# Kernel tuning notes

Measured on AMD Instinct MI355X. Metric: run time of the kernel, lower is better.

## Reference

```python
import jax, jax.numpy as jnp
import numpy as np

N_NODES = 50000
N_EDGES = 800000
D = 64
L = 3


def setup_inputs() -> dict:
    key = jax.random.key(0)
    ks = jax.random.split(key, 6)
    glorot = (6.0 / (D + D)) ** 0.5  # xavier_uniform bound for [D,D]
    return {
        "x": jax.random.normal(ks[0], (N_NODES, D), dtype=jnp.float32),
        "edge_index": jax.random.randint(ks[1], (2, N_EDGES), 0, N_NODES, dtype=jnp.int32),
        "edge_weight": jax.random.uniform(ks[2], (N_EDGES,), dtype=jnp.float32),
        "W_rel": jax.random.uniform(ks[3], (L, D, D), jnp.float32, -glorot, glorot),
        "b_rel": jnp.zeros((L, D), dtype=jnp.float32),
        "W_root": jax.random.uniform(ks[4], (L, D, D), jnp.float32, -glorot, glorot),
    }


def reference(x, edge_index, edge_weight, W_rel, b_rel, W_root):
    """myGNN_hidden.full_forward final embedding: L GraphConv(add) layers, tanh on last.
    GraphConv: h_i' = h_i @ W_root + (sum_{j->i} e_ji * h_j) @ W_rel + b_rel.
    """
    src, dst = edge_index[0], edge_index[1]
    n = x.shape[0]
    h = x
    num_layers = W_rel.shape[0]
    for i in range(num_layers):
        msg = edge_weight[:, None] * h[src]                      # [E, D] gather + scale
        agg = jax.ops.segment_sum(msg, dst, num_segments=n)      # [N, D] scatter-add
        h = agg @ W_rel[i] + b_rel[i] + h @ W_root[i]
        if i == num_layers - 1:
            h = jnp.tanh(h)
    return h
```

## Files before the change

### kernel.cpp

```cpp
#include <hip/hip_runtime.h>
#include <hip/hip_bf16.h>

#define NN 50000
#define NE 800000
#define DD 64
#define NL 3
#define NE_PAD (NE + NN * 8)

__device__ __forceinline__ float rlane(float v, int l) {
    return __int_as_float(__builtin_amdgcn_readlane(__float_as_int(v), l));
}

__global__ void hist_kernel(const int* __restrict__ dst,
                            int* __restrict__ deg,
                            int* __restrict__ rank) {
    int t = blockIdx.x * blockDim.x + threadIdx.x;
    int e = t * 4;
    if (e + 4 <= NE) {
        int4 d4 = *reinterpret_cast<const int4*>(dst + e);
        int r0 = atomicAdd(&deg[d4.x], 1);
        int r1 = atomicAdd(&deg[d4.y], 1);
        int r2 = atomicAdd(&deg[d4.z], 1);
        int r3 = atomicAdd(&deg[d4.w], 1);
        *reinterpret_cast<int4*>(rank + e) = make_int4(r0, r1, r2, r3);
    } else {
        for (int i = e; i < NE; ++i) rank[i] = atomicAdd(&deg[dst[i]], 1);
    }
}

__global__ void alloc_kernel(const int* __restrict__ deg,
                             int* __restrict__ row_start,
                             int* __restrict__ counter) {
    int n = blockIdx.x * blockDim.x + threadIdx.x;
    int lane = threadIdx.x & 63;
    int d = (n < NN) ? ((deg[n] + 7) & ~7) : 0;
    int s = d;
    #pragma unroll
    for (int off = 1; off < 64; off <<= 1) {
        int t = __shfl_up(s, off);
        if (lane >= off) s += t;
    }
    int total = __shfl(s, 63);
    int base = 0;
    if (lane == 63) base = atomicAdd(counter, total);
    base = __shfl(base, 63);
    int my = base + s - d;
    if (n < NN) row_start[n] = my;
}

__global__ void reorder_kernel(const int* __restrict__ src,
                               const int* __restrict__ dst,
                               const float* __restrict__ w,
                               const int* __restrict__ rank,
                               const int* __restrict__ row_start,
                               int2* __restrict__ e_sw) {
    int t = blockIdx.x * blockDim.x + threadIdx.x;
    int e = t * 2;
    if (e + 2 <= NE) {
        int2   s2 = *reinterpret_cast<const int2*>(src + e);
        int2   d2 = *reinterpret_cast<const int2*>(dst + e);
        float2 w2 = *reinterpret_cast<const float2*>(w + e);
        int2   r2 = *reinterpret_cast<const int2*>(rank + e);
        e_sw[row_start[d2.x] + r2.x] = make_int2(s2.x, __float_as_int(w2.x));
        e_sw[row_start[d2.y] + r2.y] = make_int2(s2.y, __float_as_int(w2.y));
    } else {
        for (int i = e; i < NE; ++i) {
            e_sw[row_start[dst[i]] + rank[i]] = make_int2(src[i], __float_as_int(w[i]));
        }
    }
}

__global__ void __launch_bounds__(256, 8)
gather_kernel(const float* __restrict__ h,
              const int* __restrict__ row_start,
              const int* __restrict__ deg,
              const int2* __restrict__ e_sw,
              float* __restrict__ agg) {
    int wid = __builtin_amdgcn_readfirstlane((int)((blockIdx.x * blockDim.x + threadIdx.x) >> 6));
    if (wid >= NN) return;
    int lane = threadIdx.x & 63;
    int beg  = __builtin_amdgcn_readfirstlane(row_start[wid]);
    int rdeg = __builtin_amdgcn_readfirstlane((deg[wid] + 7) & ~7);
    float a0=0.f,a1=0.f,a2=0.f,a3=0.f,a4=0.f,a5=0.f,a6=0.f,a7=0.f;
    for (int i = 0; i < rdeg; i += 8) {
        const int2* ep = e_sw + beg + i;
        int2 e0 = ep[0]; int2 e1 = ep[1];
        int2 e2 = ep[2]; int2 e3 = ep[3];
        int2 e4 = ep[4]; int2 e5 = ep[5];
        int2 e6 = ep[6]; int2 e7 = ep[7];
        a0 += __int_as_float(e0.y) * h[(size_t)e0.x * DD + lane];
        a1 += __int_as_float(e1.y) * h[(size_t)e1.x * DD + lane];
        a2 += __int_as_float(e2.y) * h[(size_t)e2.x * DD + lane];
        a3 += __int_as_float(e3.y) * h[(size_t)e3.x * DD + lane];
        a4 += __int_as_float(e4.y) * h[(size_t)e4.x * DD + lane];
        a5 += __int_as_float(e5.y) * h[(size_t)e5.x * DD + lane];
        a6 += __int_as_float(e6.y) * h[(size_t)e6.x * DD + lane];
        a7 += __int_as_float(e7.y) * h[(size_t)e7.x * DD + lane];
    }
    agg[(size_t)wid * DD + lane] = ((a0+a1)+(a2+a3)) + ((a4+a5)+(a6+a7));
}

template<bool LAST>
__global__ void __launch_bounds__(256, 3)
dense_kernel(const float* __restrict__ agg,
             const float* h,
             const float* __restrict__ Wrel,
             const float* __restrict__ Wroot,
             const float* __restrict__ b,
             float* hout) {
    const int lane   = threadIdx.x & 63;
    const int wgid   = __builtin_amdgcn_readfirstlane((int)((blockIdx.x * blockDim.x + threadIdx.x) >> 6));
    const int nwaves = (gridDim.x * blockDim.x) >> 6;

    float w1[DD], w2[DD];
    #pragma unroll
    for (int k = 0; k < DD; ++k) {
        w1[k] = Wrel[k * DD + lane];
        w2[k] = Wroot[k * DD + lane];
    }
    const float bias = b[lane];

    for (int n = wgid; n < NN; n += nwaves) {
        const float vagg = agg[(size_t)n * DD + lane];
        const float vh   = h[(size_t)n * DD + lane];
        float a0 = bias, a1 = 0.f, a2 = 0.f, a3 = 0.f;
        #pragma unroll
        for (int k = 0; k < DD; k += 2) {
            float sa0 = rlane(vagg, k),     sh0 = rlane(vh, k);
            float sa1 = rlane(vagg, k + 1), sh1 = rlane(vh, k + 1);
            a0 += sa0 * w1[k];
            a1 += sh0 * w2[k];
            a2 += sa1 * w1[k + 1];
            a3 += sh1 * w2[k + 1];
        }
        float r = (a0 + a1) + (a2 + a3);
        if (LAST) r = tanhf(r);
        hout[(size_t)n * DD + lane] = r;
    }
}

extern "C" void kernel_launch(void* const* d_in, const int* in_sizes, int n_in,
                              void* d_out, int out_size, void* d_ws, size_t ws_size,
                              hipStream_t stream) {
    const float* x     = (const float*)d_in[0];
    const int*   ei    = (const int*)d_in[1];
    const float* ew    = (const float*)d_in[2];
    const float* Wrel  = (const float*)d_in[3];
    const float* brel  = (const float*)d_in[4];
    const float* Wroot = (const float*)d_in[5];
    float* out = (float*)d_out;

    float* agg       = (float*)d_ws;
    float* hA        = agg + (size_t)NN * DD;
    int2*  e_sw      = (int2*)(hA + (size_t)NN * DD);
    int*   row_start = (int*)(e_sw + NE_PAD);
    int*   deg       = row_start + NN;
    int*   counter   = deg + NN;
    int*   rank      = counter + 1;

    const int* src = ei;
    const int* dst = ei + NE;

    const int hblocks = (NE / 4 + 255) / 256;
    const int rblocks = (NE / 2 + 255) / 256;
    const int ablocks = (NN + 255) / 256;
    const int gblocks = (NN * 64 + 255) / 256;
    const int dblocks = 1024;

    hipMemsetAsync(deg, 0, (size_t)(NN + 1) * sizeof(int), stream);
    hipMemsetAsync(e_sw, 0, (size_t)NE_PAD * sizeof(int2), stream);
    hist_kernel<<<hblocks, 256, 0, stream>>>(dst, deg, rank);
    alloc_kernel<<<ablocks, 256, 0, stream>>>(deg, row_start, counter);
    reorder_kernel<<<rblocks, 256, 0, stream>>>(src, dst, ew, rank, row_start, e_sw);

    gather_kernel<<<gblocks, 256, 0, stream>>>(x, row_start, deg, e_sw, agg);
    dense_kernel<false><<<dblocks, 256, 0, stream>>>(agg, x, Wrel, Wroot, brel, hA);
    gather_kernel<<<gblocks, 256, 0, stream>>>(hA, row_start, deg, e_sw, agg);
    dense_kernel<false><<<dblocks, 256, 0, stream>>>(agg, hA, Wrel + DD*DD, Wroot + DD*DD, brel + DD, hA);
    gather_kernel<<<gblocks, 256, 0, stream>>>(hA, row_start, deg, e_sw, agg);
    dense_kernel<true ><<<dblocks, 256, 0, stream>>>(agg, hA, Wrel + 2*DD*DD, Wroot + 2*DD*DD, brel + 2*DD, out);
}
```

Measured before the change: 303.5 us.

## Gather neighbor rows with float4 loads across four lane groups, pad rows to 16

The gather kernel now splits each wavefront into four 16-lane groups. Each group loads a full 64-float neighbor row with float4 loads and handles a different edge, so one wave processes 16 edges per iteration. Partial sums are combined across groups with xor shuffles, and only the first 16 lanes write the result. Row padding grows from 8 to 16 edges, which adds zero-weight padded edges for low-degree nodes (average degree 16) and enlarges the edge buffer and its memset.

```diff
diff --git a/kernel.cpp b/kernel.cpp
--- a/kernel.cpp
+++ b/kernel.cpp
@@ -5,7 +5,7 @@
 #define NE 800000
 #define DD 64
 #define NL 3
-#define NE_PAD (NE + NN * 8)
+#define NE_PAD (NE + NN * 16)
 
 __device__ __forceinline__ float rlane(float v, int l) {
     return __int_as_float(__builtin_amdgcn_readlane(__float_as_int(v), l));
@@ -33,7 +33,7 @@
                              int* __restrict__ counter) {
     int n = blockIdx.x * blockDim.x + threadIdx.x;
     int lane = threadIdx.x & 63;
-    int d = (n < NN) ? ((deg[n] + 7) & ~7) : 0;
+    int d = (n < NN) ? ((deg[n] + 15) & ~15) : 0;
     int s = d;
     #pragma unroll
     for (int off = 1; off < 64; off <<= 1) {
@@ -78,26 +78,53 @@
               float* __restrict__ agg) {
     int wid = __builtin_amdgcn_readfirstlane((int)((blockIdx.x * blockDim.x + threadIdx.x) >> 6));
     if (wid >= NN) return;
-    int lane = threadIdx.x & 63;
-    int beg  = __builtin_amdgcn_readfirstlane(row_start[wid]);
-    int rdeg = __builtin_amdgcn_readfirstlane((deg[wid] + 7) & ~7);
-    float a0=0.f,a1=0.f,a2=0.f,a3=0.f,a4=0.f,a5=0.f,a6=0.f,a7=0.f;
-    for (int i = 0; i < rdeg; i += 8) {
+    const int lane = threadIdx.x & 63;
+    const int g    = lane >> 4;
+    const int cq   = (lane & 15) << 2;
+    const int beg  = __builtin_amdgcn_readfirstlane(row_start[wid]);
+    const int rdeg = __builtin_amdgcn_readfirstlane((deg[wid] + 15) & ~15);
+
+    float ax0=0.f, ay0=0.f, az0=0.f, aw0=0.f;
+    float ax1=0.f, ay1=0.f, az1=0.f, aw1=0.f;
+    float ax2=0.f, ay2=0.f, az2=0.f, aw2=0.f;
+    float ax3=0.f, ay3=0.f, az3=0.f, aw3=0.f;
+
+    for (int i = 0; i < rdeg; i += 16) {
         const int2* ep = e_sw + beg + i;
-        int2 e0 = ep[0]; int2 e1 = ep[1];
-        int2 e2 = ep[2]; int2 e3 = ep[3];
-        int2 e4 = ep[4]; int2 e5 = ep[5];
-        int2 e6 = ep[6]; int2 e7 = ep[7];
-        a0 += __int_as_float(e0.y) * h[(size_t)e0.x * DD + lane];
-        a1 += __int_as_float(e1.y) * h[(size_t)e1.x * DD + lane];
-        a2 += __int_as_float(e2.y) * h[(size_t)e2.x * DD + lane];
-        a3 += __int_as_float(e3.y) * h[(size_t)e3.x * DD + lane];
-        a4 += __int_as_float(e4.y) * h[(size_t)e4.x * DD + lane];
-        a5 += __int_as_float(e5.y) * h[(size_t)e5.x * DD + lane];
-        a6 += __int_as_float(e6.y) * h[(size_t)e6.x * DD + lane];
-        a7 += __int_as_float(e7.y) * h[(size_t)e7.x * DD + lane];
-    }
-    agg[(size_t)wid * DD + lane] = ((a0+a1)+(a2+a3)) + ((a4+a5)+(a6+a7));
+        int2 m0 = ep[0],  m1 = ep[1],  m2 = ep[2],  m3 = ep[3];
+        int2 m4 = ep[4],  m5 = ep[5],  m6 = ep[6],  m7 = ep[7];
+        int2 m8 = ep[8],  m9 = ep[9],  m10= ep[10], m11= ep[11];
+        int2 m12= ep[12], m13= ep[13], m14= ep[14], m15= ep[15];
+
+#define SLOT(AX,AY,AZ,AW, EA,EB,EC,ED)                                          \
+        {                                                                       \
+            int  srcg = (g==0) ? EA.x : (g==1) ? EB.x : (g==2) ? EC.x : ED.x;   \
+            int  wig  = (g==0) ? EA.y : (g==1) ? EB.y : (g==2) ? EC.y : ED.y;   \
+            float wg  = __int_as_float(wig);                                    \
+            const float4 r = *reinterpret_cast<const float4*>(                  \
+                h + (size_t)srcg * DD + cq);                                    \
+            AX += wg * r.x; AY += wg * r.y; AZ += wg * r.z; AW += wg * r.w;     \
+        }
+        SLOT(ax0,ay0,az0,aw0, m0,m1,m2,m3)
+        SLOT(ax1,ay1,az1,aw1, m4,m5,m6,m7)
+        SLOT(ax2,ay2,az2,aw2, m8,m9,m10,m11)
+        SLOT(ax3,ay3,az3,aw3, m12,m13,m14,m15)
+#undef SLOT
+    }
+
+    float tx = (ax0+ax1)+(ax2+ax3);
+    float ty = (ay0+ay1)+(ay2+ay3);
+    float tz = (az0+az1)+(az2+az3);
+    float tw = (aw0+aw1)+(aw2+aw3);
+    tx += __shfl_xor(tx, 16); tx += __shfl_xor(tx, 32);
+    ty += __shfl_xor(ty, 16); ty += __shfl_xor(ty, 32);
+    tz += __shfl_xor(tz, 16); tz += __shfl_xor(tz, 32);
+    tw += __shfl_xor(tw, 16); tw += __shfl_xor(tw, 32);
+
+    if (lane < 16) {
+        float4 t = make_float4(tx, ty, tz, tw);
+        *reinterpret_cast<float4*>(agg + (size_t)wid * DD + cq) = t;
+    }
 }
 
 template<bool LAST>
```

Result: no change. 302.6 us (-0.3%).
